# Optimization experiments

Hardware: AMD Instinct MI355X
Metric: run time of the kernel (lower is better)

The kernel has to match this reference:

```python
import jax, jax.numpy as jnp
import numpy as np
from jax import lax

BS = 64    # block size
NH = 8     # attention heads
L = 12     # layers
NEG = -1e9
EPS = 1e-12  # BigBird layer_norm_eps


def gelu_new(x):
    c = 0.7978845608028654  # sqrt(2/pi)
    return 0.5 * x * (1.0 + jnp.tanh(c * (x + 0.044715 * x * x * x)))


def layer_norm(x, s, b):
    m = jnp.mean(x, axis=-1, keepdims=True)
    v = jnp.var(x, axis=-1, keepdims=True)
    return (x - m) * lax.rsqrt(v + EPS) * s + b


def block_sparse_attn(q, k, v, mask, key_blocks):
    # q,k,v: [B,H,S,hd]; mask: [B,S] (1=keep); key_blocks: [nb-2, K] block ids
    B, H, S, hd = q.shape
    nb = S // BS
    nm = nb - 2
    K = key_blocks.shape[1]
    scale = 1.0 / np.sqrt(hd)
    qb = q.reshape(B, H, nb, BS, hd)
    kb = k.reshape(B, H, nb, BS, hd)
    vb = v.reshape(B, H, nb, BS, hd)
    mb = mask.reshape(B, nb, BS)
    # middle query blocks: attend to gathered global+window+random key blocks
    q_mid = qb[:, :, 1:-1]                                   # [B,H,nm,BS,hd]
    kg = kb[:, :, key_blocks]                                # [B,H,nm,K,BS,hd]
    vg = vb[:, :, key_blocks].reshape(B, H, nm, K * BS, hd)
    mg = mb[:, key_blocks].reshape(B, 1, nm, 1, K * BS)
    s_mid = jnp.einsum('bhnqd,bhnkzd->bhnqkz', q_mid, kg).reshape(B, H, nm, BS, K * BS)
    s_mid = s_mid * scale + NEG * (1.0 - mg)
    ctx_mid = jnp.einsum('bhnqk,bhnkd->bhnqd', jax.nn.softmax(s_mid, axis=-1), vg)
    # first/last query blocks are global: full attention rows
    q_edge = jnp.stack([qb[:, :, 0], qb[:, :, -1]], axis=2)  # [B,H,2,BS,hd]
    s_edge = jnp.einsum('bhnqd,bhkd->bhnqk', q_edge, k) * scale
    s_edge = s_edge + NEG * (1.0 - mask)[:, None, None, None, :]
    ctx_edge = jnp.einsum('bhnqk,bhkd->bhnqd', jax.nn.softmax(s_edge, axis=-1), v)
    ctx = jnp.concatenate([ctx_edge[:, :, :1], ctx_mid, ctx_edge[:, :, 1:]], axis=2)
    return ctx.reshape(B, H, S, hd)


def encoder_layer(x, p, mask, key_blocks):
    Wq, bq, Wk, bk, Wv, bv, Wo, bo, l1s, l1b, Wi_, bi_, Wo2_, bo2_, l2s, l2b = p
    B, S, Hm = x.shape
    hd = Hm // NH
    def heads(t):
        return t.reshape(B, S, NH, hd).transpose(0, 2, 1, 3)
    q = heads(x @ Wq + bq)
    k = heads(x @ Wk + bk)
    v = heads(x @ Wv + bv)
    ctx = block_sparse_attn(q, k, v, mask, key_blocks)
    ctx = ctx.transpose(0, 2, 1, 3).reshape(B, S, Hm)
    x = layer_norm(x + ctx @ Wo + bo, l1s, l1b)
    ff = gelu_new(x @ Wi_ + bi_) @ Wo2_ + bo2_
    return layer_norm(x + ff, l2s, l2b)


def forward(x, proj_w, proj_b, pos_emb, tok_emb, emb_ln_s, emb_ln_b, Wq, bq, Wk, bk, Wv, bv, Wo, bo, ln1_s, ln1_b, Wi, bi, Wo2, bo2, ln2_s, ln2_b, cw1, cb1, cw2, cb2, mask, key_blocks):
    h = x @ proj_w + proj_b                 # input projection to hidden 1536
    h = h + pos_emb[None] + tok_emb         # BigBird embeddings (token_type id 0)
    h = layer_norm(h, emb_ln_s, emb_ln_b)
    stack = (Wq, bq, Wk, bk, Wv, bv, Wo, bo, ln1_s, ln1_b, Wi, bi, Wo2, bo2, ln2_s, ln2_b)
    def body(carry, p):
        return encoder_layer(carry, p, mask, key_blocks), None
    h, _ = lax.scan(jax.checkpoint(body), h, stack)
    # replaced classifier head applied per token: Linear->ReLU->Linear
    return jnp.maximum(h @ cw1 + cb1, 0.0) @ cw2 + cb2


def setup_inputs():
    key = jax.random.key(0)
    ks = iter(jax.random.split(key, 64))
    def w(*shape):
        return jax.random.normal(next(ks), shape, jnp.float32) * 0.02
    B, S, DIN, H, FF, T = 1, 4096, 1280, 1536, 3072, 256
    nb = S // BS
    # deterministic random-block plan: per middle block, 3 random blocks
    # outside {global 0, global nb-1, window i-1..i+1}
    rng = np.random.RandomState(0)
    rows = []
    for i in range(1, nb - 1):
        fixed = [0, nb - 1, i - 1, i, i + 1]
        cand = np.setdiff1d(np.arange(nb), np.array(fixed))
        rows.append(fixed + list(rng.choice(cand, 3, replace=False)))
    key_blocks = jnp.asarray(np.array(rows, dtype=np.int32))
    z = jnp.zeros
    o = jnp.ones
    return dict(
        x=jax.random.normal(next(ks), (B, S, DIN), jnp.float32),
        proj_w=w(DIN, H), proj_b=z((H,)),
        pos_emb=w(S, H), tok_emb=w(H),
        emb_ln_s=o((H,)), emb_ln_b=z((H,)),
        Wq=w(L, H, H), bq=z((L, H)), Wk=w(L, H, H), bk=z((L, H)),
        Wv=w(L, H, H), bv=z((L, H)), Wo=w(L, H, H), bo=z((L, H)),
        ln1_s=o((L, H)), ln1_b=z((L, H)),
        Wi=w(L, H, FF), bi=z((L, FF)), Wo2=w(L, FF, H), bo2=z((L, H)),
        ln2_s=o((L, H)), ln2_b=z((L, H)),
        cw1=w(H, 512), cb1=z((512,)), cw2=w(512, T), cb2=z((T,)),
        attention_mask=jnp.ones((B, S), jnp.int32),
        key_blocks=key_blocks)


def reference(x, proj_w, proj_b, pos_emb, tok_emb, emb_ln_s, emb_ln_b, Wq, bq, Wk, bk, Wv, bv, Wo, bo, ln1_s, ln1_b, Wi, bi, Wo2, bo2, ln2_s, ln2_b, cw1, cb1, cw2, cb2, attention_mask, key_blocks):
    mask = attention_mask.astype(jnp.float32)
    return forward(x, proj_w, proj_b, pos_emb, tok_emb, emb_ln_s, emb_ln_b, Wq, bq, Wk, bk, Wv, bv, Wo, bo, ln1_s, ln1_b, Wi, bi, Wo2, bo2, ln2_s, ln2_b, cw1, cb1, cw2, cb2, mask, key_blocks)
```

## Files before the change

### kernel.cpp

```cpp
#include <hip/hip_runtime.h>

typedef unsigned short u16;
typedef unsigned int u32;
typedef __bf16 bf16x8 __attribute__((ext_vector_type(8)));
typedef float f32x4 __attribute__((ext_vector_type(4)));

#define SEQ 4096
#define HM 1536
#define QKVN 4608

__device__ inline u16 f2b(float f){
  u32 u = __builtin_bit_cast(u32, f);
  return (u16)((u + 0x7fffu + ((u>>16)&1u)) >> 16);
}
__device__ inline bf16x8 ld8(const u16* p){ return *reinterpret_cast<const bf16x8*>(p); }
__device__ inline void gload16(const void* g, void* l){
  __builtin_amdgcn_global_load_lds((const __attribute__((address_space(1))) void*)g,
                                   (__attribute__((address_space(3))) void*)l, 16, 0, 0);
}

__global__ void cvt_k(const float* __restrict__ in, u16* __restrict__ outp, int n4){
  int i = blockIdx.x*256 + threadIdx.x;
  if (i < n4){
    float4 f = reinterpret_cast<const float4*>(in)[i];
    ushort4 u; u.x=f2b(f.x); u.y=f2b(f.y); u.z=f2b(f.z); u.w=f2b(f.w);
    reinterpret_cast<ushort4*>(outp)[i] = u;
  }
}

__global__ void tconv(const float* __restrict__ W, u16* __restrict__ Wt, int K, int N){
  __shared__ float tile[32][33];
  int n0 = blockIdx.x*32, k0 = blockIdx.y*32;
  int tx = threadIdx.x, ty = threadIdx.y;
  #pragma unroll
  for (int i=0;i<4;i++){
    int kk = ty + i*8;
    tile[kk][tx] = W[(size_t)(k0+kk)*N + n0 + tx];
  }
  __syncthreads();
  #pragma unroll
  for (int i=0;i<4;i++){
    int nn = ty + i*8;
    Wt[(size_t)(n0+nn)*K + k0 + tx] = f2b(tile[tx][nn]);
  }
}

__global__ void tconv3(const float* __restrict__ W0, const float* __restrict__ W1,
                       const float* __restrict__ W2, u16* __restrict__ Wt){
  __shared__ float tile[32][33];
  const float* W = (blockIdx.z==0) ? W0 : (blockIdx.z==1 ? W1 : W2);
  u16* dst = Wt + (size_t)blockIdx.z*1536*1536;
  int n0 = blockIdx.x*32, k0 = blockIdx.y*32;
  int tx = threadIdx.x, ty = threadIdx.y;
  #pragma unroll
  for (int i=0;i<4;i++){
    int kk = ty + i*8;
    tile[kk][tx] = W[(size_t)(k0+kk)*1536 + n0 + tx];
  }
  __syncthreads();
  #pragma unroll
  for (int i=0;i<4;i++){
    int nn = ty + i*8;
    dst[(size_t)(n0+nn)*1536 + k0 + tx] = f2b(tile[tx][nn]);
  }
}

__global__ void vtrans_k(const u16* __restrict__ qkv, u16* __restrict__ vt){
  __shared__ u16 tile[32][33];
  int c0 = blockIdx.x*32, s0 = blockIdx.y*32;
  int tx = threadIdx.x, ty = threadIdx.y;
  #pragma unroll
  for (int i=0;i<4;i++)
    tile[ty+i*8][tx] = qkv[(size_t)(s0+ty+i*8)*QKVN + 3072 + c0 + tx];
  __syncthreads();
  #pragma unroll
  for (int i=0;i<4;i++)
    vt[(size_t)(c0+ty+i*8)*SEQ + s0 + tx] = tile[tx][ty+i*8];
}

__global__ void concat3_k(float* __restrict__ dst, const float* __restrict__ a,
                          const float* __restrict__ b, const float* __restrict__ c){
  int i = blockIdx.x*256 + threadIdx.x;
  if (i < 1536){ dst[i]=a[i]; dst[1536+i]=b[i]; dst[3072+i]=c[i]; }
}

template<int MODE>
__global__ __launch_bounds__(256) void gemm_k(
                       const u16* __restrict__ A, const u16* __restrict__ Bt,
                       const float* __restrict__ bias, const float* __restrict__ resid,
                       const float* __restrict__ pos, const float* __restrict__ tok,
                       u16* __restrict__ outB, float* __restrict__ outF,
                       int M, int N, int K){
  __shared__ __align__(16) u16 As[128*32];
  __shared__ __align__(16) u16 Bs[128*32];
  const int t = threadIdx.x;
  const int m0 = blockIdx.y*128, n0 = blockIdx.x*128;
  const int w = t>>6, l = t&63;
  const int wm = (w>>1)*64, wn = (w&1)*64;
  const int lr = l&15, lg = l>>4;
  const int srow = w*32 + (l>>2);
  const int scol = (l&3)*8;
  const u16* Ap = A  + (size_t)(m0 + srow)*K + scol;
  const u16* Bp = Bt + (size_t)(n0 + srow)*K + scol;
  f32x4 acc[4][4] = {};

  for (int k0 = 0; k0 < K; k0 += 32){
    #pragma unroll
    for (int i=0;i<2;i++){
      gload16(Ap + (size_t)i*16*K + k0, &As[(w*2+i)*512]);
      gload16(Bp + (size_t)i*16*K + k0, &Bs[(w*2+i)*512]);
    }
    __syncthreads();
    bf16x8 af[4], bfr[4];
    #pragma unroll
    for (int i=0;i<4;i++){
      af[i]  = ld8(&As[(wm + i*16 + lr)*32 + lg*8]);
      bfr[i] = ld8(&Bs[(wn + i*16 + lr)*32 + lg*8]);
    }
    #pragma unroll
    for (int i=0;i<4;i++)
      #pragma unroll
      for (int j=0;j<4;j++)
        acc[i][j] = __builtin_amdgcn_mfma_f32_16x16x32_bf16(af[i], bfr[j], acc[i][j], 0,0,0);
    __syncthreads();
  }

  #pragma unroll
  for (int i=0;i<4;i++){
    #pragma unroll
    for (int j=0;j<4;j++){
      int col = n0 + wn + j*16 + lr;
      float bv = bias[col];
      #pragma unroll
      for (int r2=0;r2<4;r2++){
        int row = m0 + wm + i*16 + lg*4 + r2;
        float v = acc[i][j][r2] + bv;
        size_t idx = (size_t)row*N + col;
        if (MODE==0) outB[idx] = f2b(v);
        else if (MODE==1) outF[idx] = v + resid[idx];
        else if (MODE==2){
          float g = 0.5f*v*(1.f + tanhf(0.7978845608028654f*(v + 0.044715f*v*v*v)));
          outB[idx] = f2b(g);
        }
        else if (MODE==3) outB[idx] = f2b(fmaxf(v, 0.f));
        else if (MODE==4) outF[idx] = v;
        else if (MODE==5) outF[idx] = v + pos[idx] + tok[col];
      }
    }
  }
}

__global__ void ln_k(const float* __restrict__ in, const float* __restrict__ g,
                     const float* __restrict__ bta, float* __restrict__ xf,
                     u16* __restrict__ xb){
  const int row = blockIdx.x, t = threadIdx.x;
  const float2* rp = reinterpret_cast<const float2*>(in + (size_t)row*HM);
  float2 v[3]; float s=0.f, s2=0.f;
  #pragma unroll
  for (int i=0;i<3;i++){
    v[i] = rp[t + i*256];
    s += v[i].x + v[i].y; s2 += v[i].x*v[i].x + v[i].y*v[i].y;
  }
  #pragma unroll
  for (int o=32;o;o>>=1){ s += __shfl_down(s,o,64); s2 += __shfl_down(s2,o,64); }
  __shared__ float red[8];
  if ((t&63)==0){ red[t>>6]=s; red[4+(t>>6)]=s2; }
  __syncthreads();
  s = red[0]+red[1]+red[2]+red[3]; s2 = red[4]+red[5]+red[6]+red[7];
  float mean = s*(1.f/1536.f);
  float var  = s2*(1.f/1536.f) - mean*mean;
  float inv  = rsqrtf(var + 1e-12f);
  float2* xfp = reinterpret_cast<float2*>(xf + (size_t)row*HM);
  u32*    xbp = reinterpret_cast<u32*>(xb + (size_t)row*HM);
  #pragma unroll
  for (int i=0;i<3;i++){
    int c2 = t + i*256;
    float2 gg = reinterpret_cast<const float2*>(g)[c2];
    float2 bb = reinterpret_cast<const float2*>(bta)[c2];
    float y0 = (v[i].x-mean)*inv*gg.x + bb.x;
    float y1 = (v[i].y-mean)*inv*gg.y + bb.y;
    xfp[c2] = make_float2(y0, y1);
    xbp[c2] = (u32)f2b(y0) | ((u32)f2b(y1) << 16);
  }
}

__device__ inline int sp_off(int row, int colu16){
  return row*256 + ((((colu16)*2) ^ ((row&7)<<4)) >> 1);
}

__global__ __launch_bounds__(256, 2) void attn_k(
    const u16* __restrict__ qkv, const u16* __restrict__ vt,
    const int* __restrict__ kblocks, const int* __restrict__ amask,
    u16* __restrict__ ctx, float* __restrict__ pO,
    float* __restrict__ pm, float* __restrict__ pl){
  __shared__ __align__(16) u16 sQ[64][200];
  __shared__ __align__(16) u16 sP[64*256];
  __shared__ float swm[4][64];
  __shared__ float swl[4][64];
  __shared__ float s_m[64];
  __shared__ float s_l[64];
  __shared__ float s_al[64];

  const int t = threadIdx.x, w = t>>6, l = t&63;
  const int lr = l&15, lg = l>>4;
  const int b = blockIdx.x;
  int h, qb, split;
  bool partial;
  if (b < 496){ h = b/62; qb = 1 + b%62; split = 0; partial = false; }
  else { int e = b-496; split = e&7; int idx = e>>3; h = idx>>1; qb = (idx&1)?63:0; partial = true; }

  {
    const u16* qg = qkv + (size_t)(qb*64)*QKVN + h*192;
    #pragma unroll
    for (int i=0;i<6;i++){
      int idx = t + i*256;
      int row = idx/24, c8 = idx%24;
      *reinterpret_cast<int4*>(&sQ[row][c8*8]) =
        *reinterpret_cast<const int4*>(qg + (size_t)row*QKVN + c8*8);
    }
  }
  if (t < 64){ s_m[t] = -3.0e38f; s_l[t] = 0.f; }
  __syncthreads();

  f32x4 accO[4][3] = {};
  const float scale = 0.07216878364870323f;

  for (int c = 0; c < 2; ++c){
    int kb4[4];
    #pragma unroll
    for (int idx=0;idx<4;idx++)
      kb4[idx] = partial ? (split*8 + c*4 + idx) : kblocks[(qb-1)*8 + c*4 + idx];
    const int kb = kb4[w];
    const u16* kp = qkv + (size_t)(kb*64)*QKVN + 1536 + h*192;
    f32x4 acc[4][4] = {};
    #pragma unroll
    for (int d0=0; d0<192; d0+=32){
      bf16x8 aq[4], bk_[4];
      #pragma unroll
      for (int i=0;i<4;i++)  aq[i]  = ld8(&sQ[i*16+lr][d0+lg*8]);
      #pragma unroll
      for (int jn=0;jn<4;jn++) bk_[jn] = ld8(kp + (size_t)(jn*16+lr)*QKVN + d0 + lg*8);
      #pragma unroll
      for (int i=0;i<4;i++)
        #pragma unroll
        for (int jn=0;jn<4;jn++)
          acc[i][jn] = __builtin_amdgcn_mfma_f32_16x16x32_bf16(aq[i], bk_[jn], acc[i][jn], 0,0,0);
    }
    bf16x8 bvx[8][3];
    #pragma unroll
    for (int ks=0; ks<8; ks++){
      const int sb = kb4[ks>>1]*64 + (ks&1)*32 + lg*8;
      #pragma unroll
      for (int jn=0;jn<3;jn++)
        bvx[ks][jn] = ld8(vt + (size_t)(h*192 + w*48 + jn*16 + lr)*SEQ + sb);
    }
    float mcol[4];
    #pragma unroll
    for (int jn=0;jn<4;jn++)
      mcol[jn] = -1e9f*(1.f - (float)amask[kb*64 + jn*16 + lr]);
    float rmax[4][4];
    #pragma unroll
    for (int i=0;i<4;i++)
      #pragma unroll
      for (int r2=0;r2<4;r2++){
        float mx = -3.0e38f;
        #pragma unroll
        for (int jn=0;jn<4;jn++){
          float sv = acc[i][jn][r2]*scale + mcol[jn];
          acc[i][jn][r2] = sv;
          mx = fmaxf(mx, sv);
        }
        #pragma unroll
        for (int o=1;o<16;o<<=1) mx = fmaxf(mx, __shfl_xor(mx, o, 64));
        rmax[i][r2] = mx;
      }
    if (lr == 0){
      #pragma unroll
      for (int i=0;i<4;i++)
        #pragma unroll
        for (int r2=0;r2<4;r2++)
          swm[w][i*16+lg*4+r2] = rmax[i][r2];
    }
    __syncthreads();
    if (t < 64){
      float mo = s_m[t];
      float mn = fmaxf(fmaxf(fmaxf(swm[0][t], swm[1][t]), fmaxf(swm[2][t], swm[3][t])), mo);
      s_al[t] = __expf(mo - mn);
      s_m[t]  = mn;
    }
    __syncthreads();
    #pragma unroll
    for (int i=0;i<4;i++)
      #pragma unroll
      for (int r2=0;r2<4;r2++){
        const int row = i*16 + lg*4 + r2;
        const float mrow = s_m[row];
        float ssum = 0.f;
        #pragma unroll
        for (int jn=0;jn<4;jn++){
          float p = __expf(acc[i][jn][r2] - mrow);
          ssum += p;
          sP[sp_off(row, w*64 + jn*16 + lr)] = f2b(p);
        }
        #pragma unroll
        for (int o=1;o<16;o<<=1) ssum += __shfl_xor(ssum, o, 64);
        if (lr == 0) swl[w][row] = ssum;
      }
    #pragma unroll
    for (int i=0;i<4;i++)
      #pragma unroll
      for (int r2=0;r2<4;r2++){
        float a = s_al[i*16+lg*4+r2];
        #pragma unroll
        for (int jn=0;jn<3;jn++) accO[i][jn][r2] *= a;
      }
    __syncthreads();
    if (t < 64)
      s_l[t] = s_l[t]*s_al[t] + swl[0][t]+swl[1][t]+swl[2][t]+swl[3][t];
    #pragma unroll
    for (int ks=0; ks<8; ks++){
      bf16x8 ap[4];
      #pragma unroll
      for (int i=0;i<4;i++) ap[i] = ld8(&sP[sp_off(i*16+lr, ks*32 + lg*8)]);
      #pragma unroll
      for (int i=0;i<4;i++)
        #pragma unroll
        for (int jn=0;jn<3;jn++)
          accO[i][jn] = __builtin_amdgcn_mfma_f32_16x16x32_bf16(ap[i], bvx[ks][jn], accO[i][jn], 0,0,0);
    }
  }
  __syncthreads();
  if (!partial){
    #pragma unroll
    for (int i=0;i<4;i++)
      #pragma unroll
      for (int r2=0;r2<4;r2++){
        const int row = i*16+lg*4+r2;
        const float inv = 1.f / s_l[row];
        #pragma unroll
        for (int jn=0;jn<3;jn++){
          const int col = h*192 + w*48 + jn*16 + lr;
          ctx[(size_t)(qb*64+row)*HM + col] = f2b(accO[i][jn][r2] * inv);
        }
      }
  } else {
    const int e = b - 496;
    #pragma unroll
    for (int i=0;i<4;i++)
      #pragma unroll
      for (int r2=0;r2<4;r2++){
        const int row = i*16+lg*4+r2;
        #pragma unroll
        for (int jn=0;jn<3;jn++){
          const int col = w*48 + jn*16 + lr;
          pO[((size_t)e*64 + row)*192 + col] = accO[i][jn][r2];
        }
      }
    if (t < 64){ pm[e*64 + t] = s_m[t]; pl[e*64 + t] = s_l[t]; }
  }
}

__global__ void attn_comb_k(const float* __restrict__ pO, const float* __restrict__ pm,
                            const float* __restrict__ pl, u16* __restrict__ ctx){
  const int b = blockIdx.x;
  const int h = b>>1, qb = (b&1)?63:0;
  const int t = threadIdx.x;
  __shared__ float sA[8][64];
  __shared__ float sInv[64];
  if (t < 64){
    float mv[8]; float M = -3.0e38f;
    #pragma unroll
    for (int s=0;s<8;s++){ mv[s] = pm[(b*8+s)*64 + t]; M = fmaxf(M, mv[s]); }
    float L = 0.f;
    #pragma unroll
    for (int s=0;s<8;s++){
      float a = __expf(mv[s]-M);
      sA[s][t] = a;
      L += pl[(b*8+s)*64 + t]*a;
    }
    sInv[t] = 1.f/L;
  }
  __syncthreads();
  #pragma unroll
  for (int i=0;i<48;i++){
    int idx = t + i*256;
    int row = idx/192, col = idx%192;
    float acc = 0.f;
    #pragma unroll
    for (int s=0;s<8;s++)
      acc += sA[s][row] * pO[((size_t)(b*8+s)*64 + row)*192 + col];
    ctx[(size_t)(qb*64+row)*HM + h*192 + col] = f2b(acc * sInv[row]);
  }
}

extern "C" void kernel_launch(void* const* d_in, const int* in_sizes, int n_in,
                              void* d_out, int out_size, void* d_ws, size_t ws_size,
                              hipStream_t stream){
  const float* x       = (const float*)d_in[0];
  const float* proj_w  = (const float*)d_in[1];
  const float* proj_b  = (const float*)d_in[2];
  const float* pos_emb = (const float*)d_in[3];
  const float* tok_emb = (const float*)d_in[4];
  const float* embs    = (const float*)d_in[5];
  const float* embb    = (const float*)d_in[6];
  const float* Wq  = (const float*)d_in[7];
  const float* bq  = (const float*)d_in[8];
  const float* Wk  = (const float*)d_in[9];
  const float* bk  = (const float*)d_in[10];
  const float* Wv  = (const float*)d_in[11];
  const float* bv  = (const float*)d_in[12];
  const float* Wo  = (const float*)d_in[13];
  const float* bo  = (const float*)d_in[14];
  const float* l1s = (const float*)d_in[15];
  const float* l1b = (const float*)d_in[16];
  const float* Wi  = (const float*)d_in[17];
  const float* bi  = (const float*)d_in[18];
  const float* Wo2 = (const float*)d_in[19];
  const float* bo2 = (const float*)d_in[20];
  const float* l2s = (const float*)d_in[21];
  const float* l2b = (const float*)d_in[22];
  const float* cw1 = (const float*)d_in[23];
  const float* cb1 = (const float*)d_in[24];
  const float* cw2 = (const float*)d_in[25];
  const float* cb2 = (const float*)d_in[26];
  const int* amask = (const int*)d_in[27];
  const int* kblk  = (const int*)d_in[28];
  float* out = (float*)d_out;

  char* base = (char*)d_ws;
  size_t off = 0;
  auto carve = [&](size_t bytes)->char*{
    char* p = base + off; off += (bytes + 255) & ~(size_t)255; return p;
  };
  float* xf32  = (float*)carve(4096ULL*1536*4);
  float* preln = (float*)carve(4096ULL*1536*4);
  u16*   xbf   = (u16*)  carve(4096ULL*1536*2);
  u16*   xinbf = (u16*)  carve(4096ULL*1280*2);
  u16*   qkv   = (u16*)  carve(4096ULL*4608*2);
  u16*   vt    = (u16*)  carve(1536ULL*4096*2);
  u16*   ctx   = (u16*)  carve(4096ULL*1536*2);
  u16*   ff1   = (u16*)  carve(4096ULL*3072*2);
  u16*   cls1  = (u16*)  carve(4096ULL*512*2);
  u16*   wt    = (u16*)  carve(4608ULL*1536*2);
  float* b3    = (float*)carve(4608ULL*4);
  float* pO    = (float*)carve(128ULL*64*192*4);
  float* pm    = (float*)carve(128ULL*64*4);
  float* pl    = (float*)carve(128ULL*64*4);
  if (off > ws_size) return;

  const dim3 tb32(32,8);

  cvt_k<<<5120, 256, 0, stream>>>(x, xinbf, 4096*1280/4);
  tconv<<<dim3(48,40), tb32, 0, stream>>>(proj_w, wt, 1280, 1536);
  gemm_k<5><<<dim3(12,32), 256, 0, stream>>>(xinbf, wt, proj_b, nullptr, pos_emb, tok_emb,
                                             nullptr, preln, 4096, 1536, 1280);
  ln_k<<<4096, 256, 0, stream>>>(preln, embs, embb, xf32, xbf);

  for (int l = 0; l < 12; ++l){
    const float* wq  = Wq  + (size_t)l*1536*1536;
    const float* wk  = Wk  + (size_t)l*1536*1536;
    const float* wv  = Wv  + (size_t)l*1536*1536;
    const float* wo  = Wo  + (size_t)l*1536*1536;
    const float* wi  = Wi  + (size_t)l*1536*3072;
    const float* wo2 = Wo2 + (size_t)l*3072*1536;
    const float* bql = bq  + (size_t)l*1536;
    const float* bkl = bk  + (size_t)l*1536;
    const float* bvl = bv  + (size_t)l*1536;
    const float* bol = bo  + (size_t)l*1536;
    const float* bil = bi  + (size_t)l*3072;
    const float* bo2l= bo2 + (size_t)l*1536;
    const float* g1  = l1s + (size_t)l*1536;
    const float* be1 = l1b + (size_t)l*1536;
    const float* g2  = l2s + (size_t)l*1536;
    const float* be2 = l2b + (size_t)l*1536;

    tconv3<<<dim3(48,48,3), tb32, 0, stream>>>(wq, wk, wv, wt);
    concat3_k<<<6, 256, 0, stream>>>(b3, bql, bkl, bvl);
    gemm_k<0><<<dim3(36,32), 256, 0, stream>>>(xbf, wt, b3, nullptr, nullptr, nullptr,
                                               qkv, nullptr, 4096, 4608, 1536);
    vtrans_k<<<dim3(48,128), tb32, 0, stream>>>(qkv, vt);

    attn_k<<<624, 256, 0, stream>>>(qkv, vt, kblk, amask, ctx, pO, pm, pl);
    attn_comb_k<<<16, 256, 0, stream>>>(pO, pm, pl, ctx);

    tconv<<<dim3(48,48), tb32, 0, stream>>>(wo, wt, 1536, 1536);
    gemm_k<1><<<dim3(12,32), 256, 0, stream>>>(ctx, wt, bol, xf32, nullptr, nullptr,
                                               nullptr, preln, 4096, 1536, 1536);
    ln_k<<<4096, 256, 0, stream>>>(preln, g1, be1, xf32, xbf);

    tconv<<<dim3(96,48), tb32, 0, stream>>>(wi, wt, 1536, 3072);
    gemm_k<2><<<dim3(24,32), 256, 0, stream>>>(xbf, wt, bil, nullptr, nullptr, nullptr,
                                               ff1, nullptr, 4096, 3072, 1536);
    tconv<<<dim3(48,96), tb32, 0, stream>>>(wo2, wt, 3072, 1536);
    gemm_k<1><<<dim3(12,32), 256, 0, stream>>>(ff1, wt, bo2l, xf32, nullptr, nullptr,
                                               nullptr, preln, 4096, 1536, 3072);
    ln_k<<<4096, 256, 0, stream>>>(preln, g2, be2, xf32, xbf);
  }

  tconv<<<dim3(16,48), tb32, 0, stream>>>(cw1, wt, 1536, 512);
  gemm_k<3><<<dim3(4,32), 256, 0, stream>>>(xbf, wt, cb1, nullptr, nullptr, nullptr,
                                            cls1, nullptr, 4096, 512, 1536);
  tconv<<<dim3(8,16), tb32, 0, stream>>>(cw2, wt, 512, 256);
  gemm_k<4><<<dim3(2,32), 256, 0, stream>>>(cls1, wt, cb2, nullptr, nullptr, nullptr,
                                            nullptr, out, 4096, 256, 512);

  (void)in_sizes; (void)n_in; (void)out_size;
}
```

Before: 6.104 ms.

## Split every attention query block into independent key-chunk partials combined afterward

The attention kernel no longer loops over two chunks of 256 keys with an online softmax. Each workgroup now handles a single 256-key chunk and writes unnormalised partial outputs plus row max and sum. Middle blocks are split into 2 pieces, edge blocks into 16, which doubles the grid, and the combine kernel now merges all query blocks. The shared memory for Q and P is merged into one buffer and the occupancy hint is raised to 4, aiming at more parallelism and occupancy. The cost is an extra fp32 partial-output round trip through global memory for every block.

```diff
diff --git a/kernel.cpp b/kernel.cpp
--- a/kernel.cpp
+++ b/kernel.cpp
@@ -188,26 +188,30 @@
   return row*256 + ((((colu16)*2) ^ ((row&7)<<4)) >> 1);
 }
 
-__global__ __launch_bounds__(256, 2) void attn_k(
+__global__ __launch_bounds__(256, 4) void attn_k(
     const u16* __restrict__ qkv, const u16* __restrict__ vt,
     const int* __restrict__ kblocks, const int* __restrict__ amask,
-    u16* __restrict__ ctx, float* __restrict__ pO,
-    float* __restrict__ pm, float* __restrict__ pl){
-  __shared__ __align__(16) u16 sQ[64][200];
-  __shared__ __align__(16) u16 sP[64*256];
+    float* __restrict__ pO, float* __restrict__ pm, float* __restrict__ pl){
+  __shared__ __align__(16) u16 sBuf[64*256];
   __shared__ float swm[4][64];
   __shared__ float swl[4][64];
   __shared__ float s_m[64];
-  __shared__ float s_l[64];
-  __shared__ float s_al[64];
 
   const int t = threadIdx.x, w = t>>6, l = t&63;
   const int lr = l&15, lg = l>>4;
   const int b = blockIdx.x;
-  int h, qb, split;
-  bool partial;
-  if (b < 496){ h = b/62; qb = 1 + b%62; split = 0; partial = false; }
-  else { int e = b-496; split = e&7; int idx = e>>3; h = idx>>1; qb = (idx&1)?63:0; partial = true; }
+  int h, qb, kb4[4];
+  if (b < 992){
+    int m = b>>1, piece = b&1;
+    h = m/62; qb = 1 + m%62;
+    #pragma unroll
+    for (int i=0;i<4;i++) kb4[i] = kblocks[(qb-1)*8 + piece*4 + i];
+  } else {
+    int e = b-992, idx = e>>4, split = e&15;
+    h = idx>>1; qb = (idx&1)?63:0;
+    #pragma unroll
+    for (int i=0;i<4;i++) kb4[i] = split*4 + i;
+  }
 
   {
     const u16* qg = qkv + (size_t)(qb*64)*QKVN + h*192;
@@ -215,168 +219,121 @@
     for (int i=0;i<6;i++){
       int idx = t + i*256;
       int row = idx/24, c8 = idx%24;
-      *reinterpret_cast<int4*>(&sQ[row][c8*8]) =
+      *reinterpret_cast<int4*>(&sBuf[row*200 + c8*8]) =
         *reinterpret_cast<const int4*>(qg + (size_t)row*QKVN + c8*8);
     }
   }
-  if (t < 64){ s_m[t] = -3.0e38f; s_l[t] = 0.f; }
-  __syncthreads();
-
-  f32x4 accO[4][3] = {};
+  __syncthreads();
+
   const float scale = 0.07216878364870323f;
-
-  for (int c = 0; c < 2; ++c){
-    int kb4[4];
-    #pragma unroll
-    for (int idx=0;idx<4;idx++)
-      kb4[idx] = partial ? (split*8 + c*4 + idx) : kblocks[(qb-1)*8 + c*4 + idx];
-    const int kb = kb4[w];
-    const u16* kp = qkv + (size_t)(kb*64)*QKVN + 1536 + h*192;
-    f32x4 acc[4][4] = {};
-    #pragma unroll
-    for (int d0=0; d0<192; d0+=32){
-      bf16x8 aq[4], bk_[4];
-      #pragma unroll
-      for (int i=0;i<4;i++)  aq[i]  = ld8(&sQ[i*16+lr][d0+lg*8]);
-      #pragma unroll
-      for (int jn=0;jn<4;jn++) bk_[jn] = ld8(kp + (size_t)(jn*16+lr)*QKVN + d0 + lg*8);
-      #pragma unroll
-      for (int i=0;i<4;i++)
-        #pragma unroll
-        for (int jn=0;jn<4;jn++)
-          acc[i][jn] = __builtin_amdgcn_mfma_f32_16x16x32_bf16(aq[i], bk_[jn], acc[i][jn], 0,0,0);
-    }
-    bf16x8 bvx[8][3];
-    #pragma unroll
-    for (int ks=0; ks<8; ks++){
-      const int sb = kb4[ks>>1]*64 + (ks&1)*32 + lg*8;
+  const int kb = kb4[w];
+
+  const u16* kp = qkv + (size_t)(kb*64)*QKVN + 1536 + h*192;
+  f32x4 acc[4][4] = {};
+  #pragma unroll
+  for (int d0=0; d0<192; d0+=32){
+    bf16x8 aq[4], bk_[4];
+    #pragma unroll
+    for (int i=0;i<4;i++)  aq[i]  = ld8(&sBuf[(i*16+lr)*200 + d0 + lg*8]);
+    #pragma unroll
+    for (int jn=0;jn<4;jn++) bk_[jn] = ld8(kp + (size_t)(jn*16+lr)*QKVN + d0 + lg*8);
+    #pragma unroll
+    for (int i=0;i<4;i++)
+      #pragma unroll
+      for (int jn=0;jn<4;jn++)
+        acc[i][jn] = __builtin_amdgcn_mfma_f32_16x16x32_bf16(aq[i], bk_[jn], acc[i][jn], 0,0,0);
+  }
+  float mcol[4];
+  #pragma unroll
+  for (int jn=0;jn<4;jn++)
+    mcol[jn] = -1e9f*(1.f - (float)amask[kb*64 + jn*16 + lr]);
+  #pragma unroll
+  for (int i=0;i<4;i++)
+    #pragma unroll
+    for (int r2=0;r2<4;r2++){
+      float mx = -3.0e38f;
+      #pragma unroll
+      for (int jn=0;jn<4;jn++){
+        float sv = acc[i][jn][r2]*scale + mcol[jn];
+        acc[i][jn][r2] = sv;
+        mx = fmaxf(mx, sv);
+      }
+      #pragma unroll
+      for (int o=1;o<16;o<<=1) mx = fmaxf(mx, __shfl_xor(mx, o, 64));
+      if (lr == 0) swm[w][i*16+lg*4+r2] = mx;
+    }
+  __syncthreads();
+  if (t < 64)
+    s_m[t] = fmaxf(fmaxf(swm[0][t], swm[1][t]), fmaxf(swm[2][t], swm[3][t]));
+  __syncthreads();
+  #pragma unroll
+  for (int i=0;i<4;i++)
+    #pragma unroll
+    for (int r2=0;r2<4;r2++){
+      const int row = i*16 + lg*4 + r2;
+      const float mrow = s_m[row];
+      float ssum = 0.f;
+      #pragma unroll
+      for (int jn=0;jn<4;jn++){
+        float p = __expf(acc[i][jn][r2] - mrow);
+        ssum += p;
+        sBuf[sp_off(row, w*64 + jn*16 + lr)] = f2b(p);
+      }
+      #pragma unroll
+      for (int o=1;o<16;o<<=1) ssum += __shfl_xor(ssum, o, 64);
+      if (lr == 0) swl[w][row] = ssum;
+    }
+  __syncthreads();
+  f32x4 oacc[4][3] = {};
+  #pragma unroll
+  for (int ks=0; ks<8; ks++){
+    bf16x8 ap[4], bv_[3];
+    #pragma unroll
+    for (int i=0;i<4;i++) ap[i] = ld8(&sBuf[sp_off(i*16+lr, ks*32 + lg*8)]);
+    const int sb = kb4[ks>>1]*64 + (ks&1)*32 + lg*8;
+    #pragma unroll
+    for (int jn=0;jn<3;jn++)
+      bv_[jn] = ld8(vt + (size_t)(h*192 + w*48 + jn*16 + lr)*SEQ + sb);
+    #pragma unroll
+    for (int i=0;i<4;i++)
       #pragma unroll
       for (int jn=0;jn<3;jn++)
-        bvx[ks][jn] = ld8(vt + (size_t)(h*192 + w*48 + jn*16 + lr)*SEQ + sb);
-    }
-    float mcol[4];
-    #pragma unroll
-    for (int jn=0;jn<4;jn++)
-      mcol[jn] = -1e9f*(1.f - (float)amask[kb*64 + jn*16 + lr]);
-    float rmax[4][4];
-    #pragma unroll
-    for (int i=0;i<4;i++)
-      #pragma unroll
-      for (int r2=0;r2<4;r2++){
-        float mx = -3.0e38f;
-        #pragma unroll
-        for (int jn=0;jn<4;jn++){
-          float sv = acc[i][jn][r2]*scale + mcol[jn];
-          acc[i][jn][r2] = sv;
-          mx = fmaxf(mx, sv);
-        }
-        #pragma unroll
-        for (int o=1;o<16;o<<=1) mx = fmaxf(mx, __shfl_xor(mx, o, 64));
-        rmax[i][r2] = mx;
+        oacc[i][jn] = __builtin_amdgcn_mfma_f32_16x16x32_bf16(ap[i], bv_[jn], oacc[i][jn], 0,0,0);
+  }
+  #pragma unroll
+  for (int i=0;i<4;i++)
+    #pragma unroll
+    for (int r2=0;r2<4;r2++){
+      const int row = i*16+lg*4+r2;
+      #pragma unroll
+      for (int jn=0;jn<3;jn++){
+        const int col = w*48 + jn*16 + lr;
+        pO[((size_t)b*64 + row)*192 + col] = oacc[i][jn][r2];
       }
-    if (lr == 0){
-      #pragma unroll
-      for (int i=0;i<4;i++)
-        #pragma unroll
-        for (int r2=0;r2<4;r2++)
-          swm[w][i*16+lg*4+r2] = rmax[i][r2];
-    }
-    __syncthreads();
-    if (t < 64){
-      float mo = s_m[t];
-      float mn = fmaxf(fmaxf(fmaxf(swm[0][t], swm[1][t]), fmaxf(swm[2][t], swm[3][t])), mo);
-      s_al[t] = __expf(mo - mn);
-      s_m[t]  = mn;
-    }
-    __syncthreads();
-    #pragma unroll
-    for (int i=0;i<4;i++)
-      #pragma unroll
-      for (int r2=0;r2<4;r2++){
-        const int row = i*16 + lg*4 + r2;
-        const float mrow = s_m[row];
-        float ssum = 0.f;
-        #pragma unroll
-        for (int jn=0;jn<4;jn++){
-          float p = __expf(acc[i][jn][r2] - mrow);
-          ssum += p;
-          sP[sp_off(row, w*64 + jn*16 + lr)] = f2b(p);
-        }
-        #pragma unroll
-        for (int o=1;o<16;o<<=1) ssum += __shfl_xor(ssum, o, 64);
-        if (lr == 0) swl[w][row] = ssum;
-      }
-    #pragma unroll
-    for (int i=0;i<4;i++)
-      #pragma unroll
-      for (int r2=0;r2<4;r2++){
-        float a = s_al[i*16+lg*4+r2];
-        #pragma unroll
-        for (int jn=0;jn<3;jn++) accO[i][jn][r2] *= a;
-      }
-    __syncthreads();
-    if (t < 64)
-      s_l[t] = s_l[t]*s_al[t] + swl[0][t]+swl[1][t]+swl[2][t]+swl[3][t];
-    #pragma unroll
-    for (int ks=0; ks<8; ks++){
-      bf16x8 ap[4];
-      #pragma unroll
-      for (int i=0;i<4;i++) ap[i] = ld8(&sP[sp_off(i*16+lr, ks*32 + lg*8)]);
-      #pragma unroll
-      for (int i=0;i<4;i++)
-        #pragma unroll
-        for (int jn=0;jn<3;jn++)
-          accO[i][jn] = __builtin_amdgcn_mfma_f32_16x16x32_bf16(ap[i], bvx[ks][jn], accO[i][jn], 0,0,0);
-    }
-  }
-  __syncthreads();
-  if (!partial){
-    #pragma unroll
-    for (int i=0;i<4;i++)
-      #pragma unroll
-      for (int r2=0;r2<4;r2++){
-        const int row = i*16+lg*4+r2;
-        const float inv = 1.f / s_l[row];
-        #pragma unroll
-        for (int jn=0;jn<3;jn++){
-          const int col = h*192 + w*48 + jn*16 + lr;
-          ctx[(size_t)(qb*64+row)*HM + col] = f2b(accO[i][jn][r2] * inv);
-        }
-      }
-  } else {
-    const int e = b - 496;
-    #pragma unroll
-    for (int i=0;i<4;i++)
-      #pragma unroll
-      for (int r2=0;r2<4;r2++){
-        const int row = i*16+lg*4+r2;
-        #pragma unroll
-        for (int jn=0;jn<3;jn++){
-          const int col = w*48 + jn*16 + lr;
-          pO[((size_t)e*64 + row)*192 + col] = accO[i][jn][r2];
-        }
-      }
-    if (t < 64){ pm[e*64 + t] = s_m[t]; pl[e*64 + t] = s_l[t]; }
+    }
+  if (t < 64){
+    pm[b*64 + t] = s_m[t];
+    pl[b*64 + t] = swl[0][t]+swl[1][t]+swl[2][t]+swl[3][t];
   }
 }
 
 __global__ void attn_comb_k(const float* __restrict__ pO, const float* __restrict__ pm,
                             const float* __restrict__ pl, u16* __restrict__ ctx){
-  const int b = blockIdx.x;
-  const int h = b>>1, qb = (b&1)?63:0;
+  const int cb = blockIdx.x;
   const int t = threadIdx.x;
-  __shared__ float sA[8][64];
+  int h, qb, np, base;
+  if (cb < 496){ h = cb/62; qb = 1 + cb%62; np = 2;  base = 2*cb; }
+  else { int idx = cb-496; h = idx>>1; qb = (idx&1)?63:0; np = 16; base = 992 + idx*16; }
+  __shared__ float sA[16][64];
   __shared__ float sInv[64];
   if (t < 64){
-    float mv[8]; float M = -3.0e38f;
-    #pragma unroll
-    for (int s=0;s<8;s++){ mv[s] = pm[(b*8+s)*64 + t]; M = fmaxf(M, mv[s]); }
+    float M = -3.0e38f;
+    for (int s=0;s<np;s++) M = fmaxf(M, pm[(base+s)*64 + t]);
     float L = 0.f;
-    #pragma unroll
-    for (int s=0;s<8;s++){
-      float a = __expf(mv[s]-M);
+    for (int s=0;s<np;s++){
+      float a = __expf(pm[(base+s)*64 + t] - M);
       sA[s][t] = a;
-      L += pl[(b*8+s)*64 + t]*a;
+      L += pl[(base+s)*64 + t]*a;
     }
     sInv[t] = 1.f/L;
   }
@@ -386,9 +343,8 @@
     int idx = t + i*256;
     int row = idx/192, col = idx%192;
     float acc = 0.f;
-    #pragma unroll
-    for (int s=0;s<8;s++)
-      acc += sA[s][row] * pO[((size_t)(b*8+s)*64 + row)*192 + col];
+    for (int s=0;s<np;s++)
+      acc += sA[s][row] * pO[((size_t)(base+s)*64 + row)*192 + col];
     ctx[(size_t)(qb*64+row)*HM + h*192 + col] = f2b(acc * sInv[row]);
   }
 }
@@ -443,9 +399,9 @@
   u16*   cls1  = (u16*)  carve(4096ULL*512*2);
   u16*   wt    = (u16*)  carve(4608ULL*1536*2);
   float* b3    = (float*)carve(4608ULL*4);
-  float* pO    = (float*)carve(128ULL*64*192*4);
-  float* pm    = (float*)carve(128ULL*64*4);
-  float* pl    = (float*)carve(128ULL*64*4);
+  float* pO    = (float*)carve(1248ULL*64*192*4);
+  float* pm    = (float*)carve(1248ULL*64*4);
+  float* pl    = (float*)carve(1248ULL*64*4);
   if (off > ws_size) return;
 
   const dim3 tb32(32,8);
@@ -480,8 +436,8 @@
                                                qkv, nullptr, 4096, 4608, 1536);
     vtrans_k<<<dim3(48,128), tb32, 0, stream>>>(qkv, vt);
 
-    attn_k<<<624, 256, 0, stream>>>(qkv, vt, kblk, amask, ctx, pO, pm, pl);
-    attn_comb_k<<<16, 256, 0, stream>>>(pO, pm, pl, ctx);
+    attn_k<<<1248, 256, 0, stream>>>(qkv, vt, kblk, amask, pO, pm, pl);
+    attn_comb_k<<<512, 256, 0, stream>>>(pO, pm, pl, ctx);
 
     tconv<<<dim3(48,48), tb32, 0, stream>>>(wo, wt, 1536, 1536);
     gemm_k<1><<<dim3(12,32), 256, 0, stream>>>(ctx, wt, bol, xf32, nullptr, nullptr,
```

New measurement: 5.661 ms. 1.08x faster.
